# Kernel optimization log

Hardware: AMD Instinct MI355X
Metric: run time of the kernel (lower is better)

The kernel has to match this reference:

```python
import jax, jax.numpy as jnp
import numpy as np

N_HEAD = 8
LN_EPS = 1e-5


def layernorm(x, g, b):
    m = x.mean(-1, keepdims=True)
    var = x.var(-1, keepdims=True)
    return (x - m) / jnp.sqrt(var + LN_EPS) * g + b


def mha(xq, xkv, key_pad, w, b, wo, bo):
    # w: [3, D, D] (q,k,v proj), key_pad: [B, Nk] bool, True = ignore
    B, Nq, D = xq.shape
    H, dh = N_HEAD, D // N_HEAD
    q = (xq @ w[0] + b[0]).reshape(B, Nq, H, dh)
    k = (xkv @ w[1] + b[1]).reshape(B, -1, H, dh)
    v = (xkv @ w[2] + b[2]).reshape(B, -1, H, dh)
    s = jnp.einsum('bqhd,bkhd->bhqk', q, k) * (1.0 / np.float32(np.sqrt(dh)))
    s = jnp.where(key_pad[:, None, None, :], jnp.float32(-1e9), s)
    a = jax.nn.softmax(s, axis=-1)
    o = jnp.einsum('bhqk,bkhd->bqhd', a, v).reshape(B, Nq, D)
    return o @ wo + bo


def coattn_layer(v, q, v_pad, q_pad, aw, ab, awo, abo, lg, lb, fw1, fb1, fw2, fb2):
    # self-attention + residual + LN
    v_a = layernorm(v + mha(v, v, v_pad, aw[0], ab[0], awo[0], abo[0]), lg[0], lb[0])
    q_a = layernorm(q + mha(q, q, q_pad, aw[1], ab[1], awo[1], abo[1]), lg[1], lb[1])
    # cross attention: note qv_attn consumes OUTPUT of vq_attn (as in original)
    vq_out = mha(v_a, q_a, q_pad, aw[2], ab[2], awo[2], abo[2])
    qv_out = mha(q_a, vq_out, v_pad, aw[3], ab[3], awo[3], abo[3])
    v = layernorm(v + vq_out, lg[2], lb[2])
    q = layernorm(q + qv_out, lg[3], lb[3])
    # FFN (fc -> relu -> fc), residual + LN
    v = layernorm(v + (jax.nn.relu(v @ fw1[0] + fb1[0]) @ fw2[0] + fb2[0]), lg[4], lb[4])
    q = layernorm(q + (jax.nn.relu(q @ fw1[1] + fb1[1]) @ fw2[1] + fb2[1]), lg[5], lb[5])
    return v, q


def setup_inputs() -> dict:
    key = jax.random.key(0)
    B, NV, NQ, D, L = 8, 512, 512, 512, 4
    DF = 4 * D
    ks = jax.random.split(key, 12)
    sd = 0.02
    inp = {}
    inp['v'] = jax.random.normal(ks[0], (B, NV, D), jnp.float32)
    inp['q'] = jax.random.normal(ks[1], (B, NQ, D), jnp.float32)
    vm = jax.random.randint(ks[2], (B, NV), 0, 2, jnp.int32)
    qm = jax.random.randint(ks[3], (B, NQ), 0, 2, jnp.int32)
    inp['v_mask'] = vm.at[:, 0].set(1)  # ensure >=1 valid token per row
    inp['q_mask'] = qm.at[:, 0].set(1)
    inp['attn_w'] = sd * jax.random.normal(ks[4], (L, 4, 3, D, D), jnp.float32)
    inp['attn_b'] = jnp.zeros((L, 4, 3, D), jnp.float32)
    inp['attn_wo'] = sd * jax.random.normal(ks[5], (L, 4, D, D), jnp.float32)
    inp['attn_bo'] = jnp.zeros((L, 4, D), jnp.float32)
    inp['ln_g'] = jnp.ones((L, 6, D), jnp.float32)
    inp['ln_b'] = jnp.zeros((L, 6, D), jnp.float32)
    inp['ffn_w1'] = sd * jax.random.normal(ks[6], (L, 2, D, DF), jnp.float32)
    inp['ffn_b1'] = jnp.zeros((L, 2, DF), jnp.float32)
    inp['ffn_w2'] = sd * jax.random.normal(ks[7], (L, 2, DF, D), jnp.float32)
    inp['ffn_b2'] = jnp.zeros((L, 2, D), jnp.float32)
    inp['att_w'] = sd * jax.random.normal(ks[8], (D,), jnp.float32)
    inp['att_b'] = jnp.zeros((), jnp.float32)
    return inp


def reference(v, q, attn_w, attn_b, attn_wo, attn_bo, ln_g, ln_b,
              ffn_w1, ffn_b1, ffn_w2, ffn_b2, att_w, att_b, v_mask, q_mask):
    v_pad = v_mask == 0  # True = pad (original: ~v_mask.bool())
    q_pad = q_mask == 0
    L = attn_w.shape[0]
    for i in range(L):
        v, q = coattn_layer(v, q, v_pad, q_pad,
                            attn_w[i], attn_b[i], attn_wo[i], attn_bo[i],
                            ln_g[i], ln_b[i],
                            ffn_w1[i], ffn_b1[i], ffn_w2[i], ffn_b2[i])
    # att_net(v_i * q_j) is a bilinear form: sum_k v_bvk * q_bqk * w_k + bias
    s = jnp.einsum('bvk,bqk,k->bvq', v, q, att_w) + att_b
    cross_mask = v_pad[:, :, None] | q_pad[:, None, :]
    s = jnp.where(cross_mask, jnp.float32(-1e9), s)
    att_maps = jax.nn.softmax(s, axis=-1)
    v_num, q_num = v.shape[1], q.shape[1]
    seq_scale = 1.0 / np.float32(np.sqrt(v_num * q_num))
    return jnp.einsum('bvk,bvq,bqk->bk', v, att_maps, q) * seq_scale
```

## Files before the change

kernel.cpp:

```cpp
#include <hip/hip_runtime.h>
#include <hip/hip_bf16.h>

typedef __hip_bfloat16 bf16;
typedef __attribute__((ext_vector_type(8))) short short8;
typedef __attribute__((ext_vector_type(4))) short short4v;
typedef __attribute__((ext_vector_type(4))) float f32x4;

#define AS1 __attribute__((address_space(1)))
#define AS3 __attribute__((address_space(3)))

#define B_  8
#define N_  512
#define D_  512
#define H_  8
#define DH_ 64
#define DF_ 2048
#define L_  4

static __device__ __forceinline__ short bfbits(float x) {
  bf16 t = __float2bfloat16(x);
  return *reinterpret_cast<short*>(&t);
}

__global__ __launch_bounds__(256) void k_prep2(const float* __restrict__ a,
                                               float* __restrict__ fa, bf16* __restrict__ ba,
                                               const float* __restrict__ bsrc,
                                               float* __restrict__ fb, bf16* __restrict__ bb,
                                               int n) {
  int i = blockIdx.x * 256 + threadIdx.x;
  if (i < n) { float v = a[i]; fa[i] = v; ba[i] = __float2bfloat16(v); }
  else { int j = i - n; float v = bsrc[j]; fb[j] = v; bb[j] = __float2bfloat16(v); }
}

__global__ __launch_bounds__(256) void k_wt(const float* __restrict__ aw_l,
                                            const float* __restrict__ awo_l,
                                            const float* __restrict__ fw1_l,
                                            const float* __restrict__ fw2_l,
                                            bf16* __restrict__ WT)
{
  __shared__ float Ls[32][33];
  int bx = blockIdx.x;
  const float* src; bf16* dst; int R, C, tr, tc;
  if (bx < 4096) {
    int id = bx >> 8, t = bx & 255;
    int m = id >> 2, part = id & 3;
    src = (part < 3) ? (aw_l + ((long)m * 3 + part) * D_ * D_)
                     : (awo_l + (long)m * D_ * D_);
    dst = WT + (long)id * 262144; R = 512; C = 512; tr = t >> 4; tc = t & 15;
  } else if (bx < 6144) {
    int q = bx - 4096; int id = q >> 10; int t = q & 1023;
    src = fw1_l + (long)id * D_ * DF_; dst = WT + 4194304 + (long)id * 1048576;
    R = 512; C = 2048; tr = t >> 6; tc = t & 63;
  } else {
    int q = bx - 6144; int id = q >> 10; int t = q & 1023;
    src = fw2_l + (long)id * DF_ * D_; dst = WT + 6291456 + (long)id * 1048576;
    R = 2048; C = 512; tr = t >> 4; tc = t & 15;
  }
  int tt = threadIdx.x;
#pragma unroll
  for (int p = 0; p < 4; ++p) {
    int idx = tt + p * 256; int lr = idx >> 5, lc = idx & 31;
    Ls[lr][lc] = src[(long)(tr * 32 + lr) * C + tc * 32 + lc];
  }
  __syncthreads();
#pragma unroll
  for (int p = 0; p < 4; ++p) {
    int idx = tt + p * 256; int lr = idx >> 5, lc = idx & 31;
    dst[(long)(tc * 32 + lr) * R + tr * 32 + lc] = __float2bfloat16(Ls[lc][lr]);
  }
}

template<int BN>
__global__ __launch_bounds__(256, 2) void k_mfma(
    const bf16* __restrict__ A, const bf16* __restrict__ A2,
    long aS, long aB, long aH, int lda,
    const bf16* __restrict__ Bm, long bS, long bB, long bH, int ldb,
    const float* __restrict__ bias, long biasS, float scale, int relu,
    float* __restrict__ Cf, long cfS, long cfB, long cfH, int ldcf,
    bf16* __restrict__ Cb, long cbS, long cbB, long cbH, int ldcb,
    int kLen, int Hh, int zPerS, int mode, int kSplit, long pStride)
{
  constexpr int MI = (BN == 128) ? 4 : 2;
  constexpr int NI = 4;
  __shared__ short As[2 * 128 * 32];
  __shared__ short Bs[2 * BN * 32];
  int tid = threadIdx.x;
  int w = tid >> 6, lane = tid & 63;
  int z = blockIdx.z;
  int kk = 0;
  if (kSplit > 1) { kk = z % kSplit; z /= kSplit; }
  int s = z / zPerS; int zz = z - s * zPerS;
  int zb = zz / Hh, zh = zz - zb * Hh;
  int row0 = blockIdx.y * 128;
  int col0 = blockIdx.x * BN;
  const bf16* Asel = (mode == 1 && col0 >= 512) ? A2 : A;
  const bf16* Ab = Asel + s * aS + zb * aB + zh * aH + (long)kk * kLen;
  const bf16* Bb = Bm + s * bS + zb * bB + zh * bH + (long)kk * kLen;
  int rw = (BN == 128) ? ((w >> 1) * 64) : (w * 32);
  int cw = (BN == 128) ? ((w & 1) * 64) : 0;
  int quad = lane >> 4, l16 = lane & 15;

  f32x4 acc[MI][NI];
#pragma unroll
  for (int i = 0; i < MI; ++i)
#pragma unroll
    for (int j = 0; j < NI; ++j) acc[i][j] = {0.f, 0.f, 0.f, 0.f};

  for (int k0 = 0; k0 < kLen; k0 += 64) {
#pragma unroll
    for (int hf = 0; hf < 2; ++hf) {
#pragma unroll
      for (int i = 0; i < 2; ++i) {
        int o = i * 4096 + w * 1024 + lane * 16;
        int r = o >> 6;
        const bf16* g = Ab + (long)(row0 + r) * lda + k0 + hf * 32 + ((o & 63) >> 1);
        char* lp = (char*)As + hf * 8192 + i * 4096 + w * 1024;
        __builtin_amdgcn_global_load_lds((const AS1 void*)g, (AS3 void*)lp, 16, 0, 0);
      }
      constexpr int BI = (BN == 128) ? 2 : 1;
#pragma unroll
      for (int i = 0; i < BI; ++i) {
        int o = i * 4096 + w * 1024 + lane * 16;
        int r = o >> 6;
        const bf16* g = Bb + (long)(col0 + r) * ldb + k0 + hf * 32 + ((o & 63) >> 1);
        char* lp = (char*)Bs + hf * (BN * 64) + i * 4096 + w * 1024;
        __builtin_amdgcn_global_load_lds((const AS1 void*)g, (AS3 void*)lp, 16, 0, 0);
      }
    }
    __syncthreads();
#pragma unroll
    for (int hf = 0; hf < 2; ++hf) {
      short8 af[MI], bfr[NI];
#pragma unroll
      for (int mi = 0; mi < MI; ++mi)
        af[mi] = *(const short8*)&As[hf * 4096 + (rw + mi * 16 + l16) * 32 + quad * 8];
#pragma unroll
      for (int ni = 0; ni < NI; ++ni)
        bfr[ni] = *(const short8*)&Bs[hf * (BN * 32) + (cw + ni * 16 + l16) * 32 + quad * 8];
#pragma unroll
      for (int mi = 0; mi < MI; ++mi)
#pragma unroll
        for (int ni = 0; ni < NI; ++ni)
          acc[mi][ni] = __builtin_amdgcn_mfma_f32_16x16x32_bf16(af[mi], bfr[ni], acc[mi][ni], 0, 0, 0);
    }
    __syncthreads();
  }

  const float* bp = (bias && kk == 0) ? bias + s * biasS : nullptr;
#pragma unroll
  for (int mi = 0; mi < MI; ++mi)
#pragma unroll
    for (int ni = 0; ni < NI; ++ni) {
      int cg = col0 + cw + ni * 16 + l16;
      float bv = bp ? bp[cg] : 0.0f;
#pragma unroll
      for (int r = 0; r < 4; ++r) {
        int rg = row0 + rw + mi * 16 + quad * 4 + r;
        float v = acc[mi][ni][r] * scale + bv;
        if (relu) v = fmaxf(v, 0.0f);
        if (mode == 1) {
          bf16* base = Cb + s * cbS;
          if (cg < 512) base[(long)rg * 512 + cg] = __float2bfloat16(v);
          else if (cg < 1024) base[2097152 + (long)rg * 512 + (cg - 512)] = __float2bfloat16(v);
          else {
            int c2 = cg - 1024;
            base[4194304 + ((long)((rg >> 9) * 8 + (c2 >> 6)) * 64 + (c2 & 63)) * 512 + (rg & 511)]
                = __float2bfloat16(v);
          }
        } else {
          if (Cf) Cf[s * cfS + (long)kk * pStride + zb * cfB + zh * cfH + (long)rg * ldcf + cg] = v;
          if (Cb) Cb[s * cbS + zb * cbB + zh * cbH + (long)rg * ldcb + cg] = __float2bfloat16(v);
        }
      }
    }
}

__global__ __launch_bounds__(256, 2) void k_flash(
    const bf16* __restrict__ QKV, long sStride,
    const int* __restrict__ km0, const int* __restrict__ km1, float scale)
{
  __shared__ short Ks[2 * 128 * 32];
  __shared__ short Vs[4 * 64 * 32];
  __shared__ short Ps[4 * 64 * 32];
  int tid = threadIdx.x, w = tid >> 6, lane = tid & 63;
  int quad = lane >> 4, l16 = lane & 15;
  int s = blockIdx.z;
  const bf16* base = QKV + s * sStride;
  int bh = blockIdx.y, b = bh >> 3, h = bh & 7;
  int qt = blockIdx.x;
  const int* km = (s ? km1 : km0) + (b << 9);
  const bf16* Kg = base + 2097152;
  const bf16* Vt = base + 4194304;
  bf16* Og = (bf16*)base;

  int qrow = (b << 9) + (qt << 6) + (w << 4) + l16;
  short8 qf[2];
  qf[0] = *(const short8*)&base[(long)qrow * 512 + h * 64 + quad * 8];
  qf[1] = *(const short8*)&base[(long)qrow * 512 + h * 64 + 32 + quad * 8];

  float m_[4], l_[4];
  f32x4 acc_o[4];
#pragma unroll
  for (int r = 0; r < 4; ++r) { m_[r] = -3e38f; l_[r] = 0.f; }
#pragma unroll
  for (int ni = 0; ni < 4; ++ni) acc_o[ni] = {0.f, 0.f, 0.f, 0.f};

  for (int kt = 0; kt < 4; ++kt) {
    __syncthreads();
#pragma unroll
    for (int i = 0; i < 4; ++i) {
      int o = i * 4096 + w * 1024 + lane * 16;
      int kc = o >> 13, rem = o & 8191;
      int n = rem >> 6, cb = rem & 63;
      const bf16* g = Kg + ((long)((b << 9) + kt * 128 + n) << 9) + h * 64 + kc * 32 + (cb >> 1);
      char* lp = (char*)Ks + i * 4096 + w * 1024;
      __builtin_amdgcn_global_load_lds((const AS1 void*)g, (AS3 void*)lp, 16, 0, 0);
    }
#pragma unroll
    for (int i = 0; i < 4; ++i) {
      int o = i * 4096 + w * 1024 + lane * 16;
      int kc = o >> 12, rem = o & 4095;
      int d = rem >> 6, cb = rem & 63;
      const bf16* g = Vt + ((long)((bh << 6) + d) << 9) + kt * 128 + kc * 32 + (cb >> 1);
      char* lp = (char*)Vs + i * 4096 + w * 1024;
      __builtin_amdgcn_global_load_lds((const AS1 void*)g, (AS3 void*)lp, 16, 0, 0);
    }
    __syncthreads();
    f32x4 sa[8];
#pragma unroll
    for (int ni = 0; ni < 8; ++ni) sa[ni] = {0.f, 0.f, 0.f, 0.f};
#pragma unroll
    for (int kc = 0; kc < 2; ++kc)
#pragma unroll
      for (int ni = 0; ni < 8; ++ni) {
        short8 bfrag = *(const short8*)&Ks[kc * 4096 + (ni * 16 + l16) * 32 + quad * 8];
        sa[ni] = __builtin_amdgcn_mfma_f32_16x16x32_bf16(qf[kc], bfrag, sa[ni], 0, 0, 0);
      }
    float sv[8][4];
#pragma unroll
    for (int ni = 0; ni < 8; ++ni) {
      int kmv = km[kt * 128 + ni * 16 + l16];
#pragma unroll
      for (int r = 0; r < 4; ++r)
        sv[ni][r] = kmv ? sa[ni][r] * scale : -1e9f;
    }
#pragma unroll
    for (int r = 0; r < 4; ++r) {
      float rmax = sv[0][r];
#pragma unroll
      for (int ni = 1; ni < 8; ++ni) rmax = fmaxf(rmax, sv[ni][r]);
#pragma unroll
      for (int o = 1; o < 16; o <<= 1) rmax = fmaxf(rmax, __shfl_xor(rmax, o, 64));
      float newm = fmaxf(m_[r], rmax);
      float alpha = __expf(m_[r] - newm);
      float psum = 0.f;
#pragma unroll
      for (int ni = 0; ni < 8; ++ni) {
        float p = __expf(sv[ni][r] - newm);
        sv[ni][r] = p; psum += p;
      }
#pragma unroll
      for (int o = 1; o < 16; o <<= 1) psum += __shfl_xor(psum, o, 64);
      l_[r] = l_[r] * alpha + psum;
      m_[r] = newm;
#pragma unroll
      for (int ni = 0; ni < 4; ++ni) acc_o[ni][r] *= alpha;
    }
#pragma unroll
    for (int ni = 0; ni < 8; ++ni) {
      int j = ni * 16 + l16;
      short* pp = &Ps[(j >> 5) * 2048 + (w * 16 + quad * 4) * 32 + (j & 31)];
#pragma unroll
      for (int r = 0; r < 4; ++r) pp[r * 32] = bfbits(sv[ni][r]);
    }
    __syncthreads();
#pragma unroll
    for (int kcp = 0; kcp < 4; ++kcp) {
      short8 af = *(const short8*)&Ps[kcp * 2048 + (w * 16 + l16) * 32 + quad * 8];
#pragma unroll
      for (int ni = 0; ni < 4; ++ni) {
        short8 bfrag = *(const short8*)&Vs[kcp * 2048 + (ni * 16 + l16) * 32 + quad * 8];
        acc_o[ni] = __builtin_amdgcn_mfma_f32_16x16x32_bf16(af, bfrag, acc_o[ni], 0, 0, 0);
      }
    }
  }
  float linv[4];
#pragma unroll
  for (int r = 0; r < 4; ++r) linv[r] = 1.0f / l_[r];
#pragma unroll
  for (int ni = 0; ni < 4; ++ni)
#pragma unroll
    for (int r = 0; r < 4; ++r) {
      long row = (b << 9) + (qt << 6) + (w << 4) + quad * 4 + r;
      Og[row * 512 + h * 64 + ni * 16 + l16] = __float2bfloat16(acc_o[ni][r] * linv[r]);
    }
}

__global__ __launch_bounds__(256) void k_ln2(
    const float* x0, const float* g0, const float* b0, float* yf0, bf16* yb0,
    const float* x1, const float* g1, const float* b1, float* yf1, bf16* yb1,
    const float* __restrict__ P, long pstr)
{
  int sel = blockIdx.x >> 12;
  long row = blockIdx.x & 4095;
  const float* x = sel ? x1 : x0;
  const float* g = sel ? g1 : g0;
  const float* bb = sel ? b1 : b0;
  float* yf = sel ? yf1 : yf0;
  bf16* yb = sel ? yb1 : yb0;
  int t = threadIdx.x;
  const float* xr = x + row * D_;
  const float* ra = P + (sel ? 2 : 0) * pstr + row * D_;
  const float* rb = ra + pstr;
  float v0 = xr[t] + ra[t] + rb[t];
  float v1 = xr[t + 256] + ra[t + 256] + rb[t + 256];
  float s = v0 + v1;
  float ss = v0 * v0 + v1 * v1;
#pragma unroll
  for (int o = 32; o > 0; o >>= 1) {
    s += __shfl_down(s, o, 64);
    ss += __shfl_down(ss, o, 64);
  }
  __shared__ float rs[4];
  __shared__ float rss[4];
  int lane = t & 63, wid = t >> 6;
  if (lane == 0) { rs[wid] = s; rss[wid] = ss; }
  __syncthreads();
  s = rs[0] + rs[1] + rs[2] + rs[3];
  ss = rss[0] + rss[1] + rss[2] + rss[3];
  float mean = s * (1.0f / D_);
  float var = ss * (1.0f / D_) - mean * mean;
  float rstd = rsqrtf(var + 1e-5f);
  float o0 = (v0 - mean) * rstd * g[t]       + bb[t];
  float o1 = (v1 - mean) * rstd * g[t + 256] + bb[t + 256];
  if (yf) { float* yr = yf + row * D_; yr[t] = o0; yr[t + 256] = o1; }
  if (yb) { bf16* yr = yb + row * D_; yr[t] = __float2bfloat16(o0); yr[t + 256] = __float2bfloat16(o1); }
}

__global__ __launch_bounds__(256) void k_sum2bf(const float* __restrict__ a,
                                                const float* __restrict__ b,
                                                bf16* __restrict__ o)
{
  int i = (blockIdx.x * 256 + threadIdx.x) * 4;
  float4 va = *(const float4*)(a + i);
  float4 vb = *(const float4*)(b + i);
  bf16 ov[4] = { __float2bfloat16(va.x + vb.x), __float2bfloat16(va.y + vb.y),
                 __float2bfloat16(va.z + vb.z), __float2bfloat16(va.w + vb.w) };
  *(short4v*)&o[i] = *(const short4v*)ov;
}

__global__ __launch_bounds__(256) void k_softmax_x(float* __restrict__ S,
                                                   const int* __restrict__ vm,
                                                   const int* __restrict__ qm)
{
  int wrow = blockIdx.x * 4 + (threadIdx.x >> 6);
  int lane = threadIdx.x & 63;
  int b = wrow >> 9, i = wrow & 511;
  bool rowpad = (vm[(b << 9) + i] == 0);
  float* p = S + (long)wrow * 512;
  const int* qb = qm + (b << 9);
  int j0 = lane * 8;
  float4 a0 = *(const float4*)(p + j0);
  float4 a1 = *(const float4*)(p + j0 + 4);
  int4 m0 = *(const int4*)(qb + j0);
  int4 m1 = *(const int4*)(qb + j0 + 4);
  float v[8];
  v[0] = (rowpad || !m0.x) ? -1e9f : a0.x; v[1] = (rowpad || !m0.y) ? -1e9f : a0.y;
  v[2] = (rowpad || !m0.z) ? -1e9f : a0.z; v[3] = (rowpad || !m0.w) ? -1e9f : a0.w;
  v[4] = (rowpad || !m1.x) ? -1e9f : a1.x; v[5] = (rowpad || !m1.y) ? -1e9f : a1.y;
  v[6] = (rowpad || !m1.z) ? -1e9f : a1.z; v[7] = (rowpad || !m1.w) ? -1e9f : a1.w;
  float mx = v[0];
#pragma unroll
  for (int u = 1; u < 8; ++u) mx = fmaxf(mx, v[u]);
#pragma unroll
  for (int o = 1; o < 64; o <<= 1) mx = fmaxf(mx, __shfl_xor(mx, o, 64));
  float e[8], sum = 0.f;
#pragma unroll
  for (int u = 0; u < 8; ++u) { e[u] = __expf(v[u] - mx); sum += e[u]; }
#pragma unroll
  for (int o = 1; o < 64; o <<= 1) sum += __shfl_xor(sum, o, 64);
  float inv = 1.0f / sum;
  bf16 ob[8];
#pragma unroll
  for (int u = 0; u < 8; ++u) ob[u] = __float2bfloat16(e[u] * inv);
  bf16* pb = (bf16*)p;
  *(short8*)&pb[j0] = *(const short8*)ob;
}

__global__ __launch_bounds__(256) void k_vwqt(const float* __restrict__ V,
                                              const float* __restrict__ Q,
                                              const float* __restrict__ w,
                                              bf16* __restrict__ Vw, bf16* __restrict__ Qt)
{
  __shared__ float Ls[32][33];
  int bx = blockIdx.x, t = threadIdx.x;
  if (bx < 2048) {
    int i = bx * 1024 + t * 4;
    float4 v = *(const float4*)(V + i);
    int k = i & 511;
    bf16 o[4] = { __float2bfloat16(v.x * w[k]),     __float2bfloat16(v.y * w[k + 1]),
                  __float2bfloat16(v.z * w[k + 2]), __float2bfloat16(v.w * w[k + 3]) };
    *(short4v*)&Vw[i] = *(const short4v*)o;
  } else {
    int q = bx - 2048; int b = q >> 8; int tq = q & 255;
    int tr = tq >> 4, tc = tq & 15;
    const float* Qb = Q + (long)b * 262144;
    bf16* Qtb = Qt + (long)b * 262144;
#pragma unroll
    for (int p = 0; p < 4; ++p) {
      int idx = t + p * 256; int lr = idx >> 5, lc = idx & 31;
      Ls[lr][lc] = Qb[(long)(tr * 32 + lr) * 512 + tc * 32 + lc];
    }
    __syncthreads();
#pragma unroll
    for (int p = 0; p < 4; ++p) {
      int idx = t + p * 256; int lr = idx >> 5, lc = idx & 31;
      Qtb[(long)(tc * 32 + lr) * 512 + tr * 32 + lc] = __float2bfloat16(Ls[lc][lr]);
    }
  }
}

__global__ __launch_bounds__(256) void k_final_out(
    const float* __restrict__ V, const float* __restrict__ QT, float* __restrict__ out)
{
  int b = blockIdx.x >> 1;
  int k = ((blockIdx.x & 1) << 8) + threadIdx.x;
  const float* Vb = V + (long)b * N_ * D_ + k;
  const float* Tb = QT + (long)b * N_ * D_ + k;
  float acc = 0.0f;
  for (int i = 0; i < N_; ++i) acc += Vb[(long)i * D_] * Tb[(long)i * D_];
  out[b * D_ + k] = acc * (1.0f / 512.0f);
}

extern "C" void kernel_launch(void* const* d_in, const int* in_sizes, int n_in,
                              void* d_out, int out_size, void* d_ws, size_t ws_size,
                              hipStream_t stream)
{
  const float* in_v   = (const float*)d_in[0];
  const float* in_q   = (const float*)d_in[1];
  const int*   v_mask = (const int*)  d_in[2];
  const int*   q_mask = (const int*)  d_in[3];
  const float* aw  = (const float*)d_in[4];
  const float* ab  = (const float*)d_in[5];
  const float* awo = (const float*)d_in[6];
  const float* abo = (const float*)d_in[7];
  const float* lg  = (const float*)d_in[8];
  const float* lb  = (const float*)d_in[9];
  const float* fw1 = (const float*)d_in[10];
  const float* fb1 = (const float*)d_in[11];
  const float* fw2 = (const float*)d_in[12];
  const float* fb2 = (const float*)d_in[13];
  const float* atw = (const float*)d_in[14];
  const float* atb = (const float*)d_in[15];
  float* out = (float*)d_out;
  (void)atb;

  const int SZ = B_ * N_ * D_;
  char* wsb = (char*)d_ws;
  const long MB = 1024L * 1024;
  float* Vcur   = (float*)(wsb + 0 * MB);
  float* Qcur   = (float*)(wsb + 8 * MB);
  float* P0     = (float*)(wsb + 16 * MB);
  const long PSZ = 2097152;
  bf16*  WT     = (bf16*) (wsb + 48 * MB);
  bf16*  Vcur_b = (bf16*) (wsb + 64 * MB);
  bf16*  Qcur_b = (bf16*) (wsb + 68 * MB);
  bf16*  VA_b   = (bf16*) (wsb + 72 * MB);
  bf16*  QA_b   = (bf16*) (wsb + 76 * MB);
  bf16*  VQ_b   = (bf16*) (wsb + 80 * MB);
  bf16*  QKV0   = (bf16*) (wsb + 84 * MB);
  bf16*  Hid    = (bf16*) (wsb + 108 * MB);
  float* Sf     = P0;
  bf16*  Vw_b   = (bf16*) (wsb + 24 * MB);
  bf16*  Qt_b   = (bf16*) (wsb + 28 * MB);
  float* Tfin   = (float*)(wsb + 32 * MB);

  const long ZBIG = 1000000;

  k_prep2<<<16384, 256, 0, stream>>>(in_v, Vcur, Vcur_b, in_q, Qcur, Qcur_b, SZ);

  for (int l = 0; l < L_; ++l) {
    const float* lgl = lg + (long)l * 6 * D_;
    const float* lbl = lb + (long)l * 6 * D_;
    k_wt<<<8192, 256, 0, stream>>>(aw + (long)l * 12 * 262144,
                                   awo + (long)l * 4 * 262144,
                                   fw1 + (long)l * 2 * 1048576,
                                   fw2 + (long)l * 2 * 1048576, WT);
    k_mfma<128><<<dim3(12, 32, 2), 256, 0, stream>>>(
        Vcur_b, Vcur_b, 2097152, 0, 0, 512,
        WT, 1048576, 0, 0, 512,
        ab + (long)l * 4 * 1536, 1536, 1.f, 0,
        nullptr, 0, 0, 0, 0, QKV0, 6291456, 0, 0, 0,
        512, 1, 1, 1, 1, 0);
    k_flash<<<dim3(8, 64, 2), 256, 0, stream>>>(QKV0, 6291456, v_mask, q_mask, 0.125f);
    k_mfma<128><<<dim3(4, 32, 4), 256, 0, stream>>>(
        QKV0, QKV0, 6291456, 0, 0, 512,
        WT + 3 * 262144, 1048576, 0, 0, 512,
        abo + (long)l * 4 * 512, 512, 1.f, 0,
        P0, 2 * PSZ, 0, 0, 512, nullptr, 0, 0, 0, 0,
        256, 1, 1, 0, 2, PSZ);
    k_ln2<<<8192, 256, 0, stream>>>(Vcur, lgl + 0 * D_, lbl + 0 * D_, nullptr, VA_b,
                                    Qcur, lgl + 1 * D_, lbl + 1 * D_, nullptr, QA_b,
                                    P0, PSZ);
    k_mfma<128><<<dim3(12, 32, 1), 256, 0, stream>>>(
        VA_b, QA_b, 0, 0, 0, 512,
        WT + 2 * 1048576, 0, 0, 0, 512,
        ab + (long)(l * 4 + 2) * 1536, 0, 1.f, 0,
        nullptr, 0, 0, 0, 0, QKV0, 0, 0, 0, 0,
        512, 1, 1, 1, 1, 0);
    k_flash<<<dim3(8, 64, 1), 256, 0, stream>>>(QKV0, 0, q_mask, q_mask, 0.125f);
    k_mfma<64><<<dim3(8, 32, 2), 256, 0, stream>>>(
        QKV0, QKV0, 0, 0, 0, 512,
        WT + (2 * 4 + 3) * 262144, 0, 0, 0, 512,
        abo + (long)(l * 4 + 2) * 512, 0, 1.f, 0,
        P0, 0, 0, 0, 512, nullptr, 0, 0, 0, 0,
        256, 1, 1, 0, 2, PSZ);
    k_sum2bf<<<2048, 256, 0, stream>>>(P0, P0 + PSZ, VQ_b);
    k_mfma<128><<<dim3(12, 32, 1), 256, 0, stream>>>(
        QA_b, VQ_b, 0, 0, 0, 512,
        WT + 3 * 1048576, 0, 0, 0, 512,
        ab + (long)(l * 4 + 3) * 1536, 0, 1.f, 0,
        nullptr, 0, 0, 0, 0, QKV0, 0, 0, 0, 0,
        512, 1, 1, 1, 1, 0);
    k_flash<<<dim3(8, 64, 1), 256, 0, stream>>>(QKV0, 0, v_mask, v_mask, 0.125f);
    k_mfma<64><<<dim3(8, 32, 2), 256, 0, stream>>>(
        QKV0, QKV0, 0, 0, 0, 512,
        WT + (3 * 4 + 3) * 262144, 0, 0, 0, 512,
        abo + (long)(l * 4 + 3) * 512, 0, 1.f, 0,
        P0 + 2 * PSZ, 0, 0, 0, 512, nullptr, 0, 0, 0, 0,
        256, 1, 1, 0, 2, PSZ);
    k_ln2<<<8192, 256, 0, stream>>>(Vcur, lgl + 2 * D_, lbl + 2 * D_, Vcur, Vcur_b,
                                    Qcur, lgl + 3 * D_, lbl + 3 * D_, Qcur, Qcur_b,
                                    P0, PSZ);
    k_mfma<128><<<dim3(16, 32, 2), 256, 0, stream>>>(
        Vcur_b, Vcur_b, 2097152, 0, 0, 512,
        WT + 4194304, 1048576, 0, 0, 512,
        fb1 + (long)l * 2 * 2048, 2048, 1.f, 1,
        nullptr, 0, 0, 0, 0, Hid, 8388608, 0, 0, 2048,
        512, 1, 1, 0, 1, 0);
    k_mfma<128><<<dim3(4, 32, 4), 256, 0, stream>>>(
        Hid, Hid, 8388608, 0, 0, 2048,
        WT + 6291456, 1048576, 0, 0, 2048,
        fb2 + (long)l * 2 * 512, 512, 1.f, 0,
        P0, 2 * PSZ, 0, 0, 512, nullptr, 0, 0, 0, 0,
        1024, 1, 1, 0, 2, PSZ);
    k_ln2<<<8192, 256, 0, stream>>>(Vcur, lgl + 4 * D_, lbl + 4 * D_, Vcur, Vcur_b,
                                    Qcur, lgl + 5 * D_, lbl + 5 * D_, Qcur, Qcur_b,
                                    P0, PSZ);
  }

  k_vwqt<<<4096, 256, 0, stream>>>(Vcur, Qcur, atw, Vw_b, Qt_b);
  k_mfma<128><<<dim3(4, 4, 8), 256, 0, stream>>>(
      Vw_b, Vw_b, 0, 262144, 0, 512, Qcur_b, 0, 262144, 0, 512,
      nullptr, 0, 1.f, 0,
      Sf, 0, 262144, 0, 512, nullptr, 0, 0, 0, 0,
      512, 1, ZBIG, 0, 1, 0);
  k_softmax_x<<<1024, 256, 0, stream>>>(Sf, v_mask, q_mask);
  k_mfma<128><<<dim3(4, 4, 8), 256, 0, stream>>>(
      (const bf16*)Sf, (const bf16*)Sf, 0, 524288, 0, 1024, Qt_b, 0, 262144, 0, 512,
      nullptr, 0, 1.f, 0,
      Tfin, 0, 262144, 0, 512, nullptr, 0, 0, 0, 0,
      512, 1, ZBIG, 0, 1, 0);
  k_final_out<<<16, 256, 0, stream>>>(Vcur, Tfin, out);

  (void)in_sizes; (void)n_in; (void)out_size; (void)ws_size;
}
```

Baseline: 1.455 ms.

## Vectorize elementwise/LN/transpose kernels, parallelize final reduction, tune flash priorities

Switches the input prep, weight transpose, Qt transpose and LayerNorm kernels to float4 loads and 4-wide bf16 stores; LayerNorm now handles two rows per block. The final per-batch reduction, previously a 16-block serial loop over 512 rows, is split into a 256-block partial-sum kernel plus a small reduction kernel to expose more parallelism. In the flash kernel it raises wave priority around the MFMA sections and drops the barrier between writing P to LDS and reading it. That barrier removal is safe only because each wave reads just the P rows it wrote itself.

```diff
diff --git a/kernel.cpp b/kernel.cpp
--- a/kernel.cpp
+++ b/kernel.cpp
@@ -26,10 +26,16 @@
                                                float* __restrict__ fa, bf16* __restrict__ ba,
                                                const float* __restrict__ bsrc,
                                                float* __restrict__ fb, bf16* __restrict__ bb,
-                                               int n) {
-  int i = blockIdx.x * 256 + threadIdx.x;
-  if (i < n) { float v = a[i]; fa[i] = v; ba[i] = __float2bfloat16(v); }
-  else { int j = i - n; float v = bsrc[j]; fb[j] = v; bb[j] = __float2bfloat16(v); }
+                                               int n4) {
+  int g = blockIdx.x * 256 + threadIdx.x;
+  const float* s; float* f; bf16* o; long idx;
+  if (g < n4) { s = a;    f = fa; o = ba; idx = (long)g * 4; }
+  else        { s = bsrc; f = fb; o = bb; idx = (long)(g - n4) * 4; }
+  float4 v = *(const float4*)(s + idx);
+  *(float4*)(f + idx) = v;
+  bf16 ov[4] = { __float2bfloat16(v.x), __float2bfloat16(v.y),
+                 __float2bfloat16(v.z), __float2bfloat16(v.w) };
+  *(short4v*)&o[idx] = *(const short4v*)ov;
 }
 
 __global__ __launch_bounds__(256) void k_wt(const float* __restrict__ aw_l,
@@ -56,18 +62,15 @@
     src = fw2_l + (long)id * DF_ * D_; dst = WT + 6291456 + (long)id * 1048576;
     R = 2048; C = 512; tr = t >> 4; tc = t & 15;
   }
-  int tt = threadIdx.x;
-#pragma unroll
-  for (int p = 0; p < 4; ++p) {
-    int idx = tt + p * 256; int lr = idx >> 5, lc = idx & 31;
-    Ls[lr][lc] = src[(long)(tr * 32 + lr) * C + tc * 32 + lc];
-  }
+  int t = threadIdx.x;
+  int lr = t >> 3, lc0 = (t & 7) * 4;
+  float4 v = *(const float4*)(src + (long)(tr * 32 + lr) * C + tc * 32 + lc0);
+  Ls[lr][lc0] = v.x; Ls[lr][lc0 + 1] = v.y; Ls[lr][lc0 + 2] = v.z; Ls[lr][lc0 + 3] = v.w;
   __syncthreads();
-#pragma unroll
-  for (int p = 0; p < 4; ++p) {
-    int idx = tt + p * 256; int lr = idx >> 5, lc = idx & 31;
-    dst[(long)(tc * 32 + lr) * R + tr * 32 + lc] = __float2bfloat16(Ls[lc][lr]);
-  }
+  bf16 ov[4];
+#pragma unroll
+  for (int j = 0; j < 4; ++j) ov[j] = __float2bfloat16(Ls[lc0 + j][lr]);
+  *(short4v*)&dst[(long)(tc * 32 + lr) * R + tr * 32 + lc0] = *(const short4v*)ov;
 }
 
 template<int BN>
@@ -229,6 +232,7 @@
     f32x4 sa[8];
 #pragma unroll
     for (int ni = 0; ni < 8; ++ni) sa[ni] = {0.f, 0.f, 0.f, 0.f};
+    __builtin_amdgcn_s_setprio(1);
 #pragma unroll
     for (int kc = 0; kc < 2; ++kc)
 #pragma unroll
@@ -236,6 +240,7 @@
         short8 bfrag = *(const short8*)&Ks[kc * 4096 + (ni * 16 + l16) * 32 + quad * 8];
         sa[ni] = __builtin_amdgcn_mfma_f32_16x16x32_bf16(qf[kc], bfrag, sa[ni], 0, 0, 0);
       }
+    __builtin_amdgcn_s_setprio(0);
     float sv[8][4];
 #pragma unroll
     for (int ni = 0; ni < 8; ++ni) {
@@ -273,7 +278,7 @@
 #pragma unroll
       for (int r = 0; r < 4; ++r) pp[r * 32] = bfbits(sv[ni][r]);
     }
-    __syncthreads();
+    __builtin_amdgcn_s_setprio(1);
 #pragma unroll
     for (int kcp = 0; kcp < 4; ++kcp) {
       short8 af = *(const short8*)&Ps[kcp * 2048 + (w * 16 + l16) * 32 + quad * 8];
@@ -283,6 +288,7 @@
         acc_o[ni] = __builtin_amdgcn_mfma_f32_16x16x32_bf16(af, bfrag, acc_o[ni], 0, 0, 0);
       }
     }
+    __builtin_amdgcn_s_setprio(0);
   }
   float linv[4];
 #pragma unroll
@@ -301,24 +307,30 @@
     const float* x1, const float* g1, const float* b1, float* yf1, bf16* yb1,
     const float* __restrict__ P, long pstr)
 {
-  int sel = blockIdx.x >> 12;
-  long row = blockIdx.x & 4095;
-  const float* x = sel ? x1 : x0;
-  const float* g = sel ? g1 : g0;
+  int t = threadIdx.x;
+  int rh = t >> 7;
+  long row = (long)blockIdx.x * 2 + rh;
+  int sel = row >= 4096;
+  long r = row & 4095;
+  const float* x  = sel ? x1 : x0;
+  const float* g  = sel ? g1 : g0;
   const float* bb = sel ? b1 : b0;
   float* yf = sel ? yf1 : yf0;
-  bf16* yb = sel ? yb1 : yb0;
-  int t = threadIdx.x;
-  const float* xr = x + row * D_;
-  const float* ra = P + (sel ? 2 : 0) * pstr + row * D_;
+  bf16*  yb = sel ? yb1 : yb0;
+  int c = (t & 127) * 4;
+  const float* xr = x + r * D_ + c;
+  const float* ra = P + (sel ? 2 : 0) * pstr + r * D_ + c;
   const float* rb = ra + pstr;
-  float v0 = xr[t] + ra[t] + rb[t];
-  float v1 = xr[t + 256] + ra[t + 256] + rb[t + 256];
-  float s = v0 + v1;
-  float ss = v0 * v0 + v1 * v1;
+  float4 xv = *(const float4*)xr;
+  float4 av = *(const float4*)ra;
+  float4 bv = *(const float4*)rb;
+  float4 v = { xv.x + av.x + bv.x, xv.y + av.y + bv.y,
+               xv.z + av.z + bv.z, xv.w + av.w + bv.w };
+  float s  = v.x + v.y + v.z + v.w;
+  float ss = v.x * v.x + v.y * v.y + v.z * v.z + v.w * v.w;
 #pragma unroll
   for (int o = 32; o > 0; o >>= 1) {
-    s += __shfl_down(s, o, 64);
+    s  += __shfl_down(s, o, 64);
     ss += __shfl_down(ss, o, 64);
   }
   __shared__ float rs[4];
@@ -326,15 +338,23 @@
   int lane = t & 63, wid = t >> 6;
   if (lane == 0) { rs[wid] = s; rss[wid] = ss; }
   __syncthreads();
-  s = rs[0] + rs[1] + rs[2] + rs[3];
-  ss = rss[0] + rss[1] + rss[2] + rss[3];
+  s  = rs[rh * 2]  + rs[rh * 2 + 1];
+  ss = rss[rh * 2] + rss[rh * 2 + 1];
   float mean = s * (1.0f / D_);
   float var = ss * (1.0f / D_) - mean * mean;
   float rstd = rsqrtf(var + 1e-5f);
-  float o0 = (v0 - mean) * rstd * g[t]       + bb[t];
-  float o1 = (v1 - mean) * rstd * g[t + 256] + bb[t + 256];
-  if (yf) { float* yr = yf + row * D_; yr[t] = o0; yr[t + 256] = o1; }
-  if (yb) { bf16* yr = yb + row * D_; yr[t] = __float2bfloat16(o0); yr[t + 256] = __float2bfloat16(o1); }
+  float4 gg = *(const float4*)(g + c);
+  float4 b4 = *(const float4*)(bb + c);
+  float4 o4 = { (v.x - mean) * rstd * gg.x + b4.x,
+                (v.y - mean) * rstd * gg.y + b4.y,
+                (v.z - mean) * rstd * gg.z + b4.z,
+                (v.w - mean) * rstd * gg.w + b4.w };
+  if (yf) *(float4*)(yf + r * D_ + c) = o4;
+  if (yb) {
+    bf16 ov[4] = { __float2bfloat16(o4.x), __float2bfloat16(o4.y),
+                   __float2bfloat16(o4.z), __float2bfloat16(o4.w) };
+    *(short4v*)&yb[r * D_ + c] = *(const short4v*)ov;
+  }
 }
 
 __global__ __launch_bounds__(256) void k_sum2bf(const float* __restrict__ a,
@@ -406,30 +426,42 @@
     int tr = tq >> 4, tc = tq & 15;
     const float* Qb = Q + (long)b * 262144;
     bf16* Qtb = Qt + (long)b * 262144;
-#pragma unroll
-    for (int p = 0; p < 4; ++p) {
-      int idx = t + p * 256; int lr = idx >> 5, lc = idx & 31;
-      Ls[lr][lc] = Qb[(long)(tr * 32 + lr) * 512 + tc * 32 + lc];
-    }
+    int lr = t >> 3, lc0 = (t & 7) * 4;
+    float4 v = *(const float4*)(Qb + (long)(tr * 32 + lr) * 512 + tc * 32 + lc0);
+    Ls[lr][lc0] = v.x; Ls[lr][lc0 + 1] = v.y; Ls[lr][lc0 + 2] = v.z; Ls[lr][lc0 + 3] = v.w;
     __syncthreads();
-#pragma unroll
-    for (int p = 0; p < 4; ++p) {
-      int idx = t + p * 256; int lr = idx >> 5, lc = idx & 31;
-      Qtb[(long)(tc * 32 + lr) * 512 + tr * 32 + lc] = __float2bfloat16(Ls[lc][lr]);
-    }
+    bf16 ov[4];
+#pragma unroll
+    for (int j = 0; j < 4; ++j) ov[j] = __float2bfloat16(Ls[lc0 + j][lr]);
+    *(short4v*)&Qtb[(long)(tc * 32 + lr) * 512 + tr * 32 + lc0] = *(const short4v*)ov;
   }
 }
 
-__global__ __launch_bounds__(256) void k_final_out(
-    const float* __restrict__ V, const float* __restrict__ QT, float* __restrict__ out)
-{
-  int b = blockIdx.x >> 1;
-  int k = ((blockIdx.x & 1) << 8) + threadIdx.x;
-  const float* Vb = V + (long)b * N_ * D_ + k;
-  const float* Tb = QT + (long)b * N_ * D_ + k;
+__global__ __launch_bounds__(256) void k_final_part(
+    const float* __restrict__ V, const float* __restrict__ QT, float* __restrict__ Pf)
+{
+  int bx = blockIdx.x;
+  int b = bx >> 5, rem = bx & 31;
+  int kc = rem >> 4, is = rem & 15;
+  int k = (kc << 8) + threadIdx.x;
+  const float* Vb = V  + (long)b * N_ * D_ + (long)(is * 32) * D_ + k;
+  const float* Tb = QT + (long)b * N_ * D_ + (long)(is * 32) * D_ + k;
   float acc = 0.0f;
-  for (int i = 0; i < N_; ++i) acc += Vb[(long)i * D_] * Tb[(long)i * D_];
-  out[b * D_ + k] = acc * (1.0f / 512.0f);
+#pragma unroll 8
+  for (int i = 0; i < 32; ++i) acc += Vb[(long)i * D_] * Tb[(long)i * D_];
+  Pf[bx * 256 + threadIdx.x] = acc;
+}
+
+__global__ __launch_bounds__(256) void k_fred(const float* __restrict__ Pf,
+                                              float* __restrict__ out)
+{
+  int b = blockIdx.x >> 1, kc = blockIdx.x & 1;
+  int k = (kc << 8) + threadIdx.x;
+  float s = 0.0f;
+#pragma unroll
+  for (int is = 0; is < 16; ++is)
+    s += Pf[(((b << 5) | (kc << 4) | is) << 8) + threadIdx.x];
+  out[b * D_ + k] = s * (1.0f / 512.0f);
 }
 
 extern "C" void kernel_launch(void* const* d_in, const int* in_sizes, int n_in,
@@ -474,10 +506,11 @@
   bf16*  Vw_b   = (bf16*) (wsb + 24 * MB);
   bf16*  Qt_b   = (bf16*) (wsb + 28 * MB);
   float* Tfin   = (float*)(wsb + 32 * MB);
+  float* Pf     = (float*)(wsb + 41 * MB);
 
   const long ZBIG = 1000000;
 
-  k_prep2<<<16384, 256, 0, stream>>>(in_v, Vcur, Vcur_b, in_q, Qcur, Qcur_b, SZ);
+  k_prep2<<<4096, 256, 0, stream>>>(in_v, Vcur, Vcur_b, in_q, Qcur, Qcur_b, SZ / 4);
 
   for (int l = 0; l < L_; ++l) {
     const float* lgl = lg + (long)l * 6 * D_;
@@ -499,7 +532,7 @@
         abo + (long)l * 4 * 512, 512, 1.f, 0,
         P0, 2 * PSZ, 0, 0, 512, nullptr, 0, 0, 0, 0,
         256, 1, 1, 0, 2, PSZ);
-    k_ln2<<<8192, 256, 0, stream>>>(Vcur, lgl + 0 * D_, lbl + 0 * D_, nullptr, VA_b,
+    k_ln2<<<4096, 256, 0, stream>>>(Vcur, lgl + 0 * D_, lbl + 0 * D_, nullptr, VA_b,
                                     Qcur, lgl + 1 * D_, lbl + 1 * D_, nullptr, QA_b,
                                     P0, PSZ);
     k_mfma<128><<<dim3(12, 32, 1), 256, 0, stream>>>(
@@ -529,7 +562,7 @@
         abo + (long)(l * 4 + 3) * 512, 0, 1.f, 0,
         P0 + 2 * PSZ, 0, 0, 0, 512, nullptr, 0, 0, 0, 0,
         256, 1, 1, 0, 2, PSZ);
-    k_ln2<<<8192, 256, 0, stream>>>(Vcur, lgl + 2 * D_, lbl + 2 * D_, Vcur, Vcur_b,
+    k_ln2<<<4096, 256, 0, stream>>>(Vcur, lgl + 2 * D_, lbl + 2 * D_, Vcur, Vcur_b,
                                     Qcur, lgl + 3 * D_, lbl + 3 * D_, Qcur, Qcur_b,
                                     P0, PSZ);
     k_mfma<128><<<dim3(16, 32, 2), 256, 0, stream>>>(
@@ -544,7 +577,7 @@
         fb2 + (long)l * 2 * 512, 512, 1.f, 0,
         P0, 2 * PSZ, 0, 0, 512, nullptr, 0, 0, 0, 0,
         1024, 1, 1, 0, 2, PSZ);
-    k_ln2<<<8192, 256, 0, stream>>>(Vcur, lgl + 4 * D_, lbl + 4 * D_, Vcur, Vcur_b,
+    k_ln2<<<4096, 256, 0, stream>>>(Vcur, lgl + 4 * D_, lbl + 4 * D_, Vcur, Vcur_b,
                                     Qcur, lgl + 5 * D_, lbl + 5 * D_, Qcur, Qcur_b,
                                     P0, PSZ);
   }
@@ -561,7 +594,8 @@
       nullptr, 0, 1.f, 0,
       Tfin, 0, 262144, 0, 512, nullptr, 0, 0, 0, 0,
       512, 1, ZBIG, 0, 1, 0);
-  k_final_out<<<16, 256, 0, stream>>>(Vcur, Tfin, out);
+  k_final_part<<<256, 256, 0, stream>>>(Vcur, Tfin, Pf);
+  k_fred<<<16, 256, 0, stream>>>(Pf, out);
 
   (void)in_sizes; (void)n_in; (void)out_size; (void)ws_size;
 }
```

New measurement: 1.447 ms, median of 2. Within noise of the previous version (-0.6%).
